# Kernel tuning notes

Measured on AMD Instinct MI355X. Metric: run time of the kernel, lower is better.

The kernel has to match this reference:

```python
import jax, jax.numpy as jnp
import numpy as np

B = 65536
DIMS = [784, 12, 10, 8, 6, 4, 10]  # fc1..fc6 in/out dims


def setup_inputs() -> dict:
    key = jax.random.key(0)
    ks = jax.random.split(key, 1 + 2 * 6)
    inp = {"x": jax.random.normal(ks[0], (B, DIMS[0]), dtype=jnp.float32)}
    for i in range(6):
        fan_in = DIMS[i]
        bound = 1.0 / np.sqrt(fan_in)  # torch nn.Linear default init range
        inp[f"W{i+1}"] = jax.random.uniform(ks[1 + 2 * i], (fan_in, DIMS[i + 1]), jnp.float32, -bound, bound)
        inp[f"b{i+1}"] = jax.random.uniform(ks[2 + 2 * i], (DIMS[i + 1],), jnp.float32, -bound, bound)
    return inp


def reference(x, W1, b1, W2, b2, W3, b3, W4, b4, W5, b5, W6, b6):
    x = x.reshape(x.shape[0], -1)
    h1 = jnp.tanh(x @ W1 + b1)   # [B, 12]
    h2 = jnp.tanh(h1 @ W2 + b2)  # [B, 10]
    h3 = jnp.tanh(h2 @ W3 + b3)  # [B, 8]
    h4 = jnp.tanh(h3 @ W4 + b4)  # [B, 6]
    h5 = jnp.tanh(h4 @ W5 + b5)  # [B, 4]
    out = h5 @ W6 + b6           # [B, 10] logits
    return (out, h1, h2, h3, h4, h5)
```

## Files before the change

kernel.cpp:

```cpp
#include <hip/hip_runtime.h>


__device__ __forceinline__ float ftanh(float v) {
    float e = __expf(2.0f * v);
    return 1.0f - 2.0f / (e + 1.0f);
}

__global__ __launch_bounds__(256, 4)
void mlp_fused2(const float* __restrict__ x,
                const float* __restrict__ W1, const float* __restrict__ b1,
                const float* __restrict__ W2, const float* __restrict__ b2,
                const float* __restrict__ W3, const float* __restrict__ b3,
                const float* __restrict__ W4, const float* __restrict__ b4,
                const float* __restrict__ W5, const float* __restrict__ b5,
                const float* __restrict__ W6, const float* __restrict__ b6,
                float* __restrict__ out)
{
    __shared__ float4 ldsW1[2352];

    const int tid = threadIdx.x;

    const float4* w1v = (const float4*)W1;
    for (int t = tid; t < 2352; t += 256) ldsW1[t] = w1v[t];
    __syncthreads();

    const int lane = tid & 63;
    const int wave = tid >> 6;
    const int r    = lane >> 2;
    const int sub  = lane & 3;
    const int row  = (blockIdx.x << 6) + (wave << 4) + r;

    float acc[12];
#pragma unroll
    for (int j = 0; j < 12; ++j) acc[j] = 0.f;

    const float4* xrow = (const float4*)(x + (size_t)row * 784);

    for (int i = 0; i < 49; ++i) {
        float4 xv = xrow[i * 4 + sub];
        const float4* wb = ldsW1 + i * 48 + sub * 12;
#pragma unroll
        for (int dk = 0; dk < 4; ++dk) {
            float xx = (dk == 0) ? xv.x : (dk == 1) ? xv.y : (dk == 2) ? xv.z : xv.w;
            float4 w0 = wb[dk * 3 + 0];
            float4 w1 = wb[dk * 3 + 1];
            float4 w2 = wb[dk * 3 + 2];
            acc[0] += xx * w0.x;  acc[1] += xx * w0.y;  acc[2]  += xx * w0.z;  acc[3]  += xx * w0.w;
            acc[4] += xx * w1.x;  acc[5] += xx * w1.y;  acc[6]  += xx * w1.z;  acc[7]  += xx * w1.w;
            acc[8] += xx * w2.x;  acc[9] += xx * w2.y;  acc[10] += xx * w2.z;  acc[11] += xx * w2.w;
        }
    }

    float h1[12];
#pragma unroll
    for (int j = 0; j < 12; ++j) {
        float z = acc[j];
        z += __shfl_xor(z, 1);
        z += __shfl_xor(z, 2);
        h1[j] = ftanh(z + b1[j]);
    }

    float h2[10];
#pragma unroll
    for (int m = 0; m < 10; ++m) {
        float s = b2[m];
#pragma unroll
        for (int j = 0; j < 12; ++j) s += h1[j] * W2[j * 10 + m];
        h2[m] = ftanh(s);
    }

    float h3[8];
#pragma unroll
    for (int m = 0; m < 8; ++m) {
        float s = b3[m];
#pragma unroll
        for (int j = 0; j < 10; ++j) s += h2[j] * W3[j * 8 + m];
        h3[m] = ftanh(s);
    }

    float h4[6];
#pragma unroll
    for (int m = 0; m < 6; ++m) {
        float s = b4[m];
#pragma unroll
        for (int j = 0; j < 8; ++j) s += h3[j] * W4[j * 6 + m];
        h4[m] = ftanh(s);
    }

    float h5[4];
#pragma unroll
    for (int m = 0; m < 4; ++m) {
        float s = b5[m];
#pragma unroll
        for (int j = 0; j < 6; ++j) s += h4[j] * W5[j * 4 + m];
        h5[m] = ftanh(s);
    }

    float o[10];
#pragma unroll
    for (int m = 0; m < 10; ++m) {
        float s = b6[m];
#pragma unroll
        for (int j = 0; j < 4; ++j) s += h5[j] * W6[j * 10 + m];
        o[m] = s;
    }

    const size_t H1 = 655360, H2 = 1441792, H3 = 2097152, H4 = 2621440, H5 = 3014656;
    float2* po  = (float2*)(out +      (size_t)row * 10);
    float4* ph1 = (float4*)(out + H1 + (size_t)row * 12);
    float2* ph2 = (float2*)(out + H2 + (size_t)row * 10);
    float4* ph3 = (float4*)(out + H3 + (size_t)row * 8);
    float2* ph4 = (float2*)(out + H4 + (size_t)row * 6);
    float4* ph5 = (float4*)(out + H5 + (size_t)row * 4);

    if (sub == 0) {
        po[0]  = make_float2(o[0], o[1]);
        po[4]  = make_float2(o[8], o[9]);
        ph2[0] = make_float2(h2[0], h2[1]);
        ph2[4] = make_float2(h2[8], h2[9]);
        ph4[1] = make_float2(h4[2], h4[3]);
    } else if (sub == 1) {
        po[1]  = make_float2(o[2], o[3]);
        ph1[0] = make_float4(h1[0], h1[1], h1[2], h1[3]);
        ph2[1] = make_float2(h2[2], h2[3]);
        ph3[0] = make_float4(h3[0], h3[1], h3[2], h3[3]);
        ph4[2] = make_float2(h4[4], h4[5]);
    } else if (sub == 2) {
        po[2]  = make_float2(o[4], o[5]);
        ph1[1] = make_float4(h1[4], h1[5], h1[6], h1[7]);
        ph2[2] = make_float2(h2[4], h2[5]);
        ph3[1] = make_float4(h3[4], h3[5], h3[6], h3[7]);
        ph5[0] = make_float4(h5[0], h5[1], h5[2], h5[3]);
    } else {
        po[3]  = make_float2(o[6], o[7]);
        ph1[2] = make_float4(h1[8], h1[9], h1[10], h1[11]);
        ph2[3] = make_float2(h2[6], h2[7]);
        ph4[0] = make_float2(h4[0], h4[1]);
    }
}

extern "C" void kernel_launch(void* const* d_in, const int* in_sizes, int n_in,
                              void* d_out, int out_size, void* d_ws, size_t ws_size,
                              hipStream_t stream) {
    (void)in_sizes; (void)n_in; (void)d_ws; (void)ws_size; (void)out_size;
    mlp_fused2<<<1024, 256, 0, stream>>>(
        (const float*)d_in[0],
        (const float*)d_in[1],  (const float*)d_in[2],
        (const float*)d_in[3],  (const float*)d_in[4],
        (const float*)d_in[5],  (const float*)d_in[6],
        (const float*)d_in[7],  (const float*)d_in[8],
        (const float*)d_in[9],  (const float*)d_in[10],
        (const float*)d_in[11], (const float*)d_in[12],
        (float*)d_out);
}
```

Baseline: 46.53 us.

## Process two rows per thread with register prefetch of x in layer-1 GEMV

Each thread now accumulates two rows (A and B, 64 apart), so every LDS weight read is reused for two rows, halving LDS traffic per row. The next x float4 is loaded ahead into registers to overlap global loads with the FMAs. The grid is halved to 512 blocks and launch bounds lowered to 2 blocks per CU, and the tail layers are moved into a helper called once per row. The cost is higher register pressure and fewer blocks to hide memory latency on a kernel that is largely bound by reading x.

```diff
diff --git a/kernel.cpp b/kernel.cpp
--- a/kernel.cpp
+++ b/kernel.cpp
@@ -6,60 +6,15 @@
     return 1.0f - 2.0f / (e + 1.0f);
 }
 
-__global__ __launch_bounds__(256, 4)
-void mlp_fused2(const float* __restrict__ x,
-                const float* __restrict__ W1, const float* __restrict__ b1,
-                const float* __restrict__ W2, const float* __restrict__ b2,
-                const float* __restrict__ W3, const float* __restrict__ b3,
-                const float* __restrict__ W4, const float* __restrict__ b4,
-                const float* __restrict__ W5, const float* __restrict__ b5,
-                const float* __restrict__ W6, const float* __restrict__ b6,
-                float* __restrict__ out)
+__device__ __forceinline__ void tiny_layers_and_store(
+        const float (&h1)[12], int row, int sub,
+        const float* __restrict__ W2, const float* __restrict__ b2,
+        const float* __restrict__ W3, const float* __restrict__ b3,
+        const float* __restrict__ W4, const float* __restrict__ b4,
+        const float* __restrict__ W5, const float* __restrict__ b5,
+        const float* __restrict__ W6, const float* __restrict__ b6,
+        float* __restrict__ out)
 {
-    __shared__ float4 ldsW1[2352];
-
-    const int tid = threadIdx.x;
-
-    const float4* w1v = (const float4*)W1;
-    for (int t = tid; t < 2352; t += 256) ldsW1[t] = w1v[t];
-    __syncthreads();
-
-    const int lane = tid & 63;
-    const int wave = tid >> 6;
-    const int r    = lane >> 2;
-    const int sub  = lane & 3;
-    const int row  = (blockIdx.x << 6) + (wave << 4) + r;
-
-    float acc[12];
-#pragma unroll
-    for (int j = 0; j < 12; ++j) acc[j] = 0.f;
-
-    const float4* xrow = (const float4*)(x + (size_t)row * 784);
-
-    for (int i = 0; i < 49; ++i) {
-        float4 xv = xrow[i * 4 + sub];
-        const float4* wb = ldsW1 + i * 48 + sub * 12;
-#pragma unroll
-        for (int dk = 0; dk < 4; ++dk) {
-            float xx = (dk == 0) ? xv.x : (dk == 1) ? xv.y : (dk == 2) ? xv.z : xv.w;
-            float4 w0 = wb[dk * 3 + 0];
-            float4 w1 = wb[dk * 3 + 1];
-            float4 w2 = wb[dk * 3 + 2];
-            acc[0] += xx * w0.x;  acc[1] += xx * w0.y;  acc[2]  += xx * w0.z;  acc[3]  += xx * w0.w;
-            acc[4] += xx * w1.x;  acc[5] += xx * w1.y;  acc[6]  += xx * w1.z;  acc[7]  += xx * w1.w;
-            acc[8] += xx * w2.x;  acc[9] += xx * w2.y;  acc[10] += xx * w2.z;  acc[11] += xx * w2.w;
-        }
-    }
-
-    float h1[12];
-#pragma unroll
-    for (int j = 0; j < 12; ++j) {
-        float z = acc[j];
-        z += __shfl_xor(z, 1);
-        z += __shfl_xor(z, 2);
-        h1[j] = ftanh(z + b1[j]);
-    }
-
     float h2[10];
 #pragma unroll
     for (int m = 0; m < 10; ++m) {
@@ -68,7 +23,6 @@
         for (int j = 0; j < 12; ++j) s += h1[j] * W2[j * 10 + m];
         h2[m] = ftanh(s);
     }
-
     float h3[8];
 #pragma unroll
     for (int m = 0; m < 8; ++m) {
@@ -77,7 +31,6 @@
         for (int j = 0; j < 10; ++j) s += h2[j] * W3[j * 8 + m];
         h3[m] = ftanh(s);
     }
-
     float h4[6];
 #pragma unroll
     for (int m = 0; m < 6; ++m) {
@@ -86,7 +39,6 @@
         for (int j = 0; j < 8; ++j) s += h3[j] * W4[j * 6 + m];
         h4[m] = ftanh(s);
     }
-
     float h5[4];
 #pragma unroll
     for (int m = 0; m < 4; ++m) {
@@ -95,7 +47,6 @@
         for (int j = 0; j < 6; ++j) s += h4[j] * W5[j * 4 + m];
         h5[m] = ftanh(s);
     }
-
     float o[10];
 #pragma unroll
     for (int m = 0; m < 10; ++m) {
@@ -139,11 +90,103 @@
     }
 }
 
+__global__ __launch_bounds__(256, 2)
+void mlp_fused3(const float* __restrict__ x,
+                const float* __restrict__ W1, const float* __restrict__ b1,
+                const float* __restrict__ W2, const float* __restrict__ b2,
+                const float* __restrict__ W3, const float* __restrict__ b3,
+                const float* __restrict__ W4, const float* __restrict__ b4,
+                const float* __restrict__ W5, const float* __restrict__ b5,
+                const float* __restrict__ W6, const float* __restrict__ b6,
+                float* __restrict__ out)
+{
+    __shared__ float4 ldsW1[2352];
+
+    const int tid = threadIdx.x;
+
+    const float4* w1v = (const float4*)W1;
+    for (int t = tid; t < 2352; t += 256) ldsW1[t] = w1v[t];
+    __syncthreads();
+
+    const int lane = tid & 63;
+    const int wave = tid >> 6;
+    const int r    = lane >> 2;
+    const int sub  = lane & 3;
+    const int rowA = (blockIdx.x << 7) + (wave << 4) + r;
+    const int rowB = rowA + 64;
+
+    float accA[12], accB[12];
+#pragma unroll
+    for (int j = 0; j < 12; ++j) { accA[j] = 0.f; accB[j] = 0.f; }
+
+    const float4* xrowA = (const float4*)(x + (size_t)rowA * 784);
+    const float4* xrowB = (const float4*)(x + (size_t)rowB * 784);
+
+    float4 curA = xrowA[sub];
+    float4 curB = xrowB[sub];
+
+#pragma unroll 2
+    for (int i = 0; i < 48; ++i) {
+        float4 nxtA = xrowA[(i + 1) * 4 + sub];
+        float4 nxtB = xrowB[(i + 1) * 4 + sub];
+        const float4* wb = &ldsW1[i * 48 + sub * 12];
+#pragma unroll
+        for (int dk = 0; dk < 4; ++dk) {
+            float xa = (dk == 0) ? curA.x : (dk == 1) ? curA.y : (dk == 2) ? curA.z : curA.w;
+            float xb = (dk == 0) ? curB.x : (dk == 1) ? curB.y : (dk == 2) ? curB.z : curB.w;
+            float4 w0 = wb[dk * 3 + 0];
+            float4 w1 = wb[dk * 3 + 1];
+            float4 w2 = wb[dk * 3 + 2];
+            accA[0] += xa * w0.x;  accA[1] += xa * w0.y;  accA[2]  += xa * w0.z;  accA[3]  += xa * w0.w;
+            accA[4] += xa * w1.x;  accA[5] += xa * w1.y;  accA[6]  += xa * w1.z;  accA[7]  += xa * w1.w;
+            accA[8] += xa * w2.x;  accA[9] += xa * w2.y;  accA[10] += xa * w2.z;  accA[11] += xa * w2.w;
+            accB[0] += xb * w0.x;  accB[1] += xb * w0.y;  accB[2]  += xb * w0.z;  accB[3]  += xb * w0.w;
+            accB[4] += xb * w1.x;  accB[5] += xb * w1.y;  accB[6]  += xb * w1.z;  accB[7]  += xb * w1.w;
+            accB[8] += xb * w2.x;  accB[9] += xb * w2.y;  accB[10] += xb * w2.z;  accB[11] += xb * w2.w;
+        }
+        curA = nxtA;
+        curB = nxtB;
+    }
+    {
+        const float4* wb = &ldsW1[48 * 48 + sub * 12];
+#pragma unroll
+        for (int dk = 0; dk < 4; ++dk) {
+            float xa = (dk == 0) ? curA.x : (dk == 1) ? curA.y : (dk == 2) ? curA.z : curA.w;
+            float xb = (dk == 0) ? curB.x : (dk == 1) ? curB.y : (dk == 2) ? curB.z : curB.w;
+            float4 w0 = wb[dk * 3 + 0];
+            float4 w1 = wb[dk * 3 + 1];
+            float4 w2 = wb[dk * 3 + 2];
+            accA[0] += xa * w0.x;  accA[1] += xa * w0.y;  accA[2]  += xa * w0.z;  accA[3]  += xa * w0.w;
+            accA[4] += xa * w1.x;  accA[5] += xa * w1.y;  accA[6]  += xa * w1.z;  accA[7]  += xa * w1.w;
+            accA[8] += xa * w2.x;  accA[9] += xa * w2.y;  accA[10] += xa * w2.z;  accA[11] += xa * w2.w;
+            accB[0] += xb * w0.x;  accB[1] += xb * w0.y;  accB[2]  += xb * w0.z;  accB[3]  += xb * w0.w;
+            accB[4] += xb * w1.x;  accB[5] += xb * w1.y;  accB[6]  += xb * w1.z;  accB[7]  += xb * w1.w;
+            accB[8] += xb * w2.x;  accB[9] += xb * w2.y;  accB[10] += xb * w2.z;  accB[11] += xb * w2.w;
+        }
+    }
+
+    float h1A[12], h1B[12];
+#pragma unroll
+    for (int j = 0; j < 12; ++j) {
+        float za = accA[j];
+        za += __shfl_xor(za, 1);
+        za += __shfl_xor(za, 2);
+        h1A[j] = ftanh(za + b1[j]);
+        float zb = accB[j];
+        zb += __shfl_xor(zb, 1);
+        zb += __shfl_xor(zb, 2);
+        h1B[j] = ftanh(zb + b1[j]);
+    }
+
+    tiny_layers_and_store(h1A, rowA, sub, W2, b2, W3, b3, W4, b4, W5, b5, W6, b6, out);
+    tiny_layers_and_store(h1B, rowB, sub, W2, b2, W3, b3, W4, b4, W5, b5, W6, b6, out);
+}
+
 extern "C" void kernel_launch(void* const* d_in, const int* in_sizes, int n_in,
                               void* d_out, int out_size, void* d_ws, size_t ws_size,
                               hipStream_t stream) {
     (void)in_sizes; (void)n_in; (void)d_ws; (void)ws_size; (void)out_size;
-    mlp_fused2<<<1024, 256, 0, stream>>>(
+    mlp_fused3<<<512, 256, 0, stream>>>(
         (const float*)d_in[0],
         (const float*)d_in[1],  (const float*)d_in[2],
         (const float*)d_in[3],  (const float*)d_in[4],
```

Measured after the change: 52.37 us. 1.13x slower.

## Store W1 in LDS as packed bf16 and prefetch x rows two iterations ahead

Applied to the files above, without the earlier changes.

Each block now converts W1 to bf16 with round-to-nearest-even while staging it into shared memory, which halves LDS footprint and read traffic in the first-layer dot-product loop. The x row loads are software-pipelined two iterations ahead to hide global latency. The bf16 rounding of weights lowers first-layer accuracy and may exceed tolerances, and the unpacking shifts add ALU work.

```diff
diff --git a/kernel.cpp b/kernel.cpp
--- a/kernel.cpp
+++ b/kernel.cpp
@@ -6,8 +6,16 @@
     return 1.0f - 2.0f / (e + 1.0f);
 }
 
+__device__ __forceinline__ uint32_t bfpack(float lo, float hi) {
+    uint32_t ul = __float_as_uint(lo);
+    uint32_t uh = __float_as_uint(hi);
+    ul += 0x7fffu + ((ul >> 16) & 1u);
+    uh += 0x7fffu + ((uh >> 16) & 1u);
+    return (ul >> 16) | (uh & 0xffff0000u);
+}
+
 __global__ __launch_bounds__(256, 4)
-void mlp_fused2(const float* __restrict__ x,
+void mlp_fused4(const float* __restrict__ x,
                 const float* __restrict__ W1, const float* __restrict__ b1,
                 const float* __restrict__ W2, const float* __restrict__ b2,
                 const float* __restrict__ W3, const float* __restrict__ b3,
@@ -16,12 +24,15 @@
                 const float* __restrict__ W6, const float* __restrict__ b6,
                 float* __restrict__ out)
 {
-    __shared__ float4 ldsW1[2352];
+    __shared__ uint32_t ldsW[4704];
 
     const int tid = threadIdx.x;
 
-    const float4* w1v = (const float4*)W1;
-    for (int t = tid; t < 2352; t += 256) ldsW1[t] = w1v[t];
+    const float2* w1v = (const float2*)W1;
+    for (int t = tid; t < 4704; t += 256) {
+        float2 p = w1v[t];
+        ldsW[t] = bfpack(p.x, p.y);
+    }
     __syncthreads();
 
     const int lane = tid & 63;
@@ -35,20 +46,33 @@
     for (int j = 0; j < 12; ++j) acc[j] = 0.f;
 
     const float4* xrow = (const float4*)(x + (size_t)row * 784);
+    const uint4*  wq   = (const uint4*)ldsW;
+
+    float4 f0 = xrow[sub];
+    float4 f1 = xrow[4 + sub];
 
     for (int i = 0; i < 49; ++i) {
-        float4 xv = xrow[i * 4 + sub];
-        const float4* wb = ldsW1 + i * 48 + sub * 12;
+        float4 f2 = (i < 47) ? xrow[(i + 2) * 4 + sub] : f0;
+
+        uint4 q[6];
+#pragma unroll
+        for (int c = 0; c < 6; ++c) q[c] = wq[i * 24 + sub * 6 + c];
+
 #pragma unroll
         for (int dk = 0; dk < 4; ++dk) {
-            float xx = (dk == 0) ? xv.x : (dk == 1) ? xv.y : (dk == 2) ? xv.z : xv.w;
-            float4 w0 = wb[dk * 3 + 0];
-            float4 w1 = wb[dk * 3 + 1];
-            float4 w2 = wb[dk * 3 + 2];
-            acc[0] += xx * w0.x;  acc[1] += xx * w0.y;  acc[2]  += xx * w0.z;  acc[3]  += xx * w0.w;
-            acc[4] += xx * w1.x;  acc[5] += xx * w1.y;  acc[6]  += xx * w1.z;  acc[7]  += xx * w1.w;
-            acc[8] += xx * w2.x;  acc[9] += xx * w2.y;  acc[10] += xx * w2.z;  acc[11] += xx * w2.w;
+            float xx = (dk == 0) ? f0.x : (dk == 1) ? f0.y : (dk == 2) ? f0.z : f0.w;
+#pragma unroll
+            for (int c = 0; c < 6; ++c) {
+                int m = 6 * dk + c;
+                uint32_t u = (m & 3) == 0 ? q[m >> 2].x :
+                             (m & 3) == 1 ? q[m >> 2].y :
+                             (m & 3) == 2 ? q[m >> 2].z : q[m >> 2].w;
+                acc[2 * c]     += xx * __uint_as_float(u << 16);
+                acc[2 * c + 1] += xx * __uint_as_float(u);
+            }
         }
+        f0 = f1;
+        f1 = f2;
     }
 
     float h1[12];
@@ -68,7 +92,6 @@
         for (int j = 0; j < 12; ++j) s += h1[j] * W2[j * 10 + m];
         h2[m] = ftanh(s);
     }
-
     float h3[8];
 #pragma unroll
     for (int m = 0; m < 8; ++m) {
@@ -77,7 +100,6 @@
         for (int j = 0; j < 10; ++j) s += h2[j] * W3[j * 8 + m];
         h3[m] = ftanh(s);
     }
-
     float h4[6];
 #pragma unroll
     for (int m = 0; m < 6; ++m) {
@@ -86,7 +108,6 @@
         for (int j = 0; j < 8; ++j) s += h3[j] * W4[j * 6 + m];
         h4[m] = ftanh(s);
     }
-
     float h5[4];
 #pragma unroll
     for (int m = 0; m < 4; ++m) {
@@ -95,7 +116,6 @@
         for (int j = 0; j < 6; ++j) s += h4[j] * W5[j * 4 + m];
         h5[m] = ftanh(s);
     }
-
     float o[10];
 #pragma unroll
     for (int m = 0; m < 10; ++m) {
@@ -143,7 +163,7 @@
                               void* d_out, int out_size, void* d_ws, size_t ws_size,
                               hipStream_t stream) {
     (void)in_sizes; (void)n_in; (void)d_ws; (void)ws_size; (void)out_size;
-    mlp_fused2<<<1024, 256, 0, stream>>>(
+    mlp_fused4<<<1024, 256, 0, stream>>>(
         (const float*)d_in[0],
         (const float*)d_in[1],  (const float*)d_in[2],
         (const float*)d_in[3],  (const float*)d_in[4],
```

Measured after the change: 57.59 us. 1.24x slower.

## Split K across waves with scalar W1 loads and LDS reduction

Applied to the files above, without the earlier changes.

Removes the per-block staging of W1 into LDS. Each wave now handles a quarter of the 784-wide K dimension for all 64 rows, one row per lane. Because the wave index is made uniform, W1 is read directly from global memory as uniform (likely scalar) loads, and x loads are software-prefetched one chunk ahead. Partial sums go through a small LDS buffer and are combined with shuffles, trading the large LDS fill and its barrier for a small reduction, at the cost of strided, less coalesced per-lane x row accesses.

```diff
diff --git a/kernel.cpp b/kernel.cpp
--- a/kernel.cpp
+++ b/kernel.cpp
@@ -7,7 +7,7 @@
 }
 
 __global__ __launch_bounds__(256, 4)
-void mlp_fused2(const float* __restrict__ x,
+void mlp_fused5(const float* __restrict__ x,
                 const float* __restrict__ W1, const float* __restrict__ b1,
                 const float* __restrict__ W2, const float* __restrict__ b2,
                 const float* __restrict__ W3, const float* __restrict__ b3,
@@ -16,45 +16,69 @@
                 const float* __restrict__ W6, const float* __restrict__ b6,
                 float* __restrict__ out)
 {
-    __shared__ float4 ldsW1[2352];
+    __shared__ float lds[64][4][13];
 
-    const int tid = threadIdx.x;
-
-    const float4* w1v = (const float4*)W1;
-    for (int t = tid; t < 2352; t += 256) ldsW1[t] = w1v[t];
-    __syncthreads();
-
+    const int tid  = threadIdx.x;
+    const int wave = __builtin_amdgcn_readfirstlane(tid >> 6);
     const int lane = tid & 63;
-    const int wave = tid >> 6;
-    const int r    = lane >> 2;
-    const int sub  = lane & 3;
-    const int row  = (blockIdx.x << 6) + (wave << 4) + r;
+    const int row0 = blockIdx.x << 6;
 
     float acc[12];
 #pragma unroll
     for (int j = 0; j < 12; ++j) acc[j] = 0.f;
 
-    const float4* xrow = (const float4*)(x + (size_t)row * 784);
+    const float4* xv4 = (const float4*)(x + (size_t)(row0 + lane) * 784 + wave * 196);
+    const float*  w1p = W1 + wave * 196 * 12;
 
-    for (int i = 0; i < 49; ++i) {
-        float4 xv = xrow[i * 4 + sub];
-        const float4* wb = ldsW1 + i * 48 + sub * 12;
+    float4 c0 = xv4[0], c1 = xv4[1], c2 = xv4[2], c3 = xv4[3];
+
+#define FMA16(wkbase)                                                          \
+    do {                                                                       \
+        const float* wk = (wkbase);                                            \
+        _Pragma("unroll")                                                      \
+        for (int dk = 0; dk < 16; ++dk) {                                      \
+            float xx = (dk >> 2) == 0 ? ((dk & 3) == 0 ? c0.x : (dk & 3) == 1 ? c0.y : (dk & 3) == 2 ? c0.z : c0.w) \
+                     : (dk >> 2) == 1 ? ((dk & 3) == 0 ? c1.x : (dk & 3) == 1 ? c1.y : (dk & 3) == 2 ? c1.z : c1.w) \
+                     : (dk >> 2) == 2 ? ((dk & 3) == 0 ? c2.x : (dk & 3) == 1 ? c2.y : (dk & 3) == 2 ? c2.z : c2.w) \
+                     :                  ((dk & 3) == 0 ? c3.x : (dk & 3) == 1 ? c3.y : (dk & 3) == 2 ? c3.z : c3.w); \
+            _Pragma("unroll")                                                  \
+            for (int j = 0; j < 12; ++j) acc[j] += xx * wk[dk * 12 + j];       \
+        }                                                                      \
+    } while (0)
+
+    for (int t = 0; t < 11; ++t) {
+        float4 n0 = xv4[t * 4 + 4];
+        float4 n1 = xv4[t * 4 + 5];
+        float4 n2 = xv4[t * 4 + 6];
+        float4 n3 = xv4[t * 4 + 7];
+        FMA16(w1p + t * 192);
+        c0 = n0; c1 = n1; c2 = n2; c3 = n3;
+    }
+    float4 tl = xv4[48];
+    FMA16(w1p + 11 * 192);
+    {
+        const float* wk = w1p + 2304;
 #pragma unroll
         for (int dk = 0; dk < 4; ++dk) {
-            float xx = (dk == 0) ? xv.x : (dk == 1) ? xv.y : (dk == 2) ? xv.z : xv.w;
-            float4 w0 = wb[dk * 3 + 0];
-            float4 w1 = wb[dk * 3 + 1];
-            float4 w2 = wb[dk * 3 + 2];
-            acc[0] += xx * w0.x;  acc[1] += xx * w0.y;  acc[2]  += xx * w0.z;  acc[3]  += xx * w0.w;
-            acc[4] += xx * w1.x;  acc[5] += xx * w1.y;  acc[6]  += xx * w1.z;  acc[7]  += xx * w1.w;
-            acc[8] += xx * w2.x;  acc[9] += xx * w2.y;  acc[10] += xx * w2.z;  acc[11] += xx * w2.w;
+            float xx = dk == 0 ? tl.x : dk == 1 ? tl.y : dk == 2 ? tl.z : tl.w;
+#pragma unroll
+            for (int j = 0; j < 12; ++j) acc[j] += xx * wk[dk * 12 + j];
         }
     }
+#undef FMA16
+
+#pragma unroll
+    for (int j = 0; j < 12; ++j) lds[lane][wave][j] = acc[j];
+    __syncthreads();
+
+    const int r   = tid >> 2;
+    const int sub = tid & 3;
+    const int row = row0 + r;
 
     float h1[12];
 #pragma unroll
     for (int j = 0; j < 12; ++j) {
-        float z = acc[j];
+        float z = lds[r][sub][j];
         z += __shfl_xor(z, 1);
         z += __shfl_xor(z, 2);
         h1[j] = ftanh(z + b1[j]);
@@ -68,7 +92,6 @@
         for (int j = 0; j < 12; ++j) s += h1[j] * W2[j * 10 + m];
         h2[m] = ftanh(s);
     }
-
     float h3[8];
 #pragma unroll
     for (int m = 0; m < 8; ++m) {
@@ -77,7 +100,6 @@
         for (int j = 0; j < 10; ++j) s += h2[j] * W3[j * 8 + m];
         h3[m] = ftanh(s);
     }
-
     float h4[6];
 #pragma unroll
     for (int m = 0; m < 6; ++m) {
@@ -86,7 +108,6 @@
         for (int j = 0; j < 8; ++j) s += h3[j] * W4[j * 6 + m];
         h4[m] = ftanh(s);
     }
-
     float h5[4];
 #pragma unroll
     for (int m = 0; m < 4; ++m) {
@@ -95,7 +116,6 @@
         for (int j = 0; j < 6; ++j) s += h4[j] * W5[j * 4 + m];
         h5[m] = ftanh(s);
     }
-
     float o[10];
 #pragma unroll
     for (int m = 0; m < 10; ++m) {
@@ -143,7 +163,7 @@
                               void* d_out, int out_size, void* d_ws, size_t ws_size,
                               hipStream_t stream) {
     (void)in_sizes; (void)n_in; (void)d_ws; (void)ws_size; (void)out_size;
-    mlp_fused2<<<1024, 256, 0, stream>>>(
+    mlp_fused5<<<1024, 256, 0, stream>>>(
         (const float*)d_in[0],
         (const float*)d_in[1],  (const float*)d_in[2],
         (const float*)d_in[3],  (const float*)d_in[4],
```

After: 53.23 us. 14.4% more time.
